# Performance work log

Measured on AMD Instinct MI355X. Metric: run time of the kernel, lower is better.

Reference implementation:

```python
import jax, jax.numpy as jnp
import numpy as np
import math

N = 50000        # nodes
DEG = 16         # regular out-degree -> E = N*DEG edges, grouped by source node
B = 64           # graphs in batch
F = 128          # num_node_features
H = 128          # nhid == enhid
RATIO = 0.5      # edge_ratio
NUM_CONVS = 3
E = N * DEG


def setup_inputs() -> dict:
    key = jax.random.key(0)
    ks = jax.random.split(key, 18)
    s = 0.05
    x = jax.random.normal(ks[0], (N, F), jnp.float32)
    edge_src = jnp.repeat(jnp.arange(N, dtype=jnp.int32), DEG)          # sorted by src
    edge_dst = jax.random.randint(ks[1], (E,), 0, N, jnp.int32)
    batch = ((jnp.arange(N) * B) // N).astype(jnp.int32)                 # sorted graph ids
    edge_attr = jnp.ones((E, 1), jnp.float32)                            # edge_attr=None branch
    inp = {"x": x, "edge_attr": edge_attr, "edge_src": edge_src,
           "edge_dst": edge_dst, "batch": batch}
    # GCNConv weights: [F->H, H->H, H->H]
    inp["W_gcn0"] = jax.random.normal(ks[2], (F, H), jnp.float32) * s
    inp["b_gcn0"] = jnp.zeros((H,), jnp.float32)
    inp["W_gcn1"] = jax.random.normal(ks[3], (H, H), jnp.float32) * s
    inp["b_gcn1"] = jnp.zeros((H,), jnp.float32)
    inp["W_gcn2"] = jax.random.normal(ks[4], (H, H), jnp.float32) * s
    inp["b_gcn2"] = jnp.zeros((H,), jnp.float32)
    # EGNN edge convs: [1->H, H->H]
    inp["W_eg0"] = jax.random.normal(ks[5], (1, H), jnp.float32) * s
    inp["b_eg0"] = jnp.zeros((H,), jnp.float32)
    inp["W_eg1"] = jax.random.normal(ks[6], (H, H), jnp.float32) * s
    inp["b_eg1"] = jnp.zeros((H,), jnp.float32)
    # score convs: [H->1, H->1]
    inp["W_sc0"] = jax.random.normal(ks[7], (H, 1), jnp.float32) * s
    inp["b_sc0"] = jnp.zeros((1,), jnp.float32)
    inp["W_sc1"] = jax.random.normal(ks[8], (H, 1), jnp.float32) * s
    inp["b_sc1"] = jnp.zeros((1,), jnp.float32)
    return inp


def _gcn(x, src, dst, ew, W, b):
    # PyG GCNConv: add self-loops (weight 1), symmetric deg normalization, aggregate at dst.
    n = x.shape[0]
    loop = jnp.arange(n, dtype=src.dtype)
    src2 = jnp.concatenate([src, loop])
    dst2 = jnp.concatenate([dst, loop])
    ew2 = jnp.concatenate([ew, jnp.ones((n,), ew.dtype)])
    deg = jax.ops.segment_sum(ew2, dst2, n)
    dinv = jnp.where(deg > 0, jax.lax.rsqrt(jnp.maximum(deg, 1e-12)), 0.0)
    norm = dinv[src2] * dinv[dst2] * ew2                                  # [E+n]
    msg = (x @ W)[src2] * norm[:, None]                                    # gather + scale
    return jax.ops.segment_sum(msg, dst2, n) + b                           # scatter-add


def _egnn(e, src, W, b):
    # Edge conv: scatter edge features to their source node, gather back, linear map.
    agg = jax.ops.segment_sum(e, src, N)
    return agg[src] @ W + b


def _pool(h, batch):
    gmax = jax.ops.segment_max(h, batch, B)
    gsum = jax.ops.segment_sum(h, batch, B)
    cnt = jax.ops.segment_sum(jnp.ones((h.shape[0],), h.dtype), batch, B)
    gmean = gsum / cnt[:, None]
    return jnp.concatenate([gmax, gmean, gsum], axis=1)                    # [B, 3H]


def reference(x, edge_attr, edge_src, edge_dst, batch,
              W_gcn0, b_gcn0, W_gcn1, b_gcn1, W_gcn2, b_gcn2,
              W_eg0, b_eg0, W_eg1, b_eg1, W_sc0, b_sc0, W_sc1, b_sc1):
    gW = [W_gcn0, W_gcn1, W_gcn2]
    gb = [b_gcn0, b_gcn1, b_gcn2]
    eW = [W_eg0, W_eg1]
    eb = [b_eg0, b_eg1]
    sW = [W_sc0, W_sc1]
    sb = [b_sc0, b_sc1]
    src, dst = edge_src, edge_dst
    deg = DEG
    ew = jnp.ones((src.shape[0],), jnp.float32)
    h = x
    ea = edge_attr
    xs = jnp.zeros((B, 3 * H), jnp.float32)
    for i in range(NUM_CONVS):
        h = jax.nn.relu(_gcn(h, src, dst, ew, gW[i], gb[i]))
        if i < NUM_CONVS - 1:
            ea = jax.nn.relu(_egnn(ea, src, eW[i], eb[i]))
            score = jnp.tanh(_egnn(ea, src, sW[i], sb[i])[:, 0])           # [E_cur]
            k = math.ceil(RATIO * deg)                                      # per-src-node top-k
            vals, idx = jax.lax.top_k(score.reshape(N, deg), k)             # [N,k]
            dst = jnp.take_along_axis(dst.reshape(N, deg), idx, axis=1).reshape(-1)
            flat = (jnp.arange(N)[:, None] * deg + idx).reshape(-1)
            ea = ea[flat]
            src = jnp.repeat(jnp.arange(N, dtype=src.dtype), k)
            ew = jnp.clip(vals.reshape(-1), 0.0, 1.0)
            deg = k
        xs = xs + _pool(h, batch)
    return xs
```

## Files before the change

### kernel.cpp

```cpp
#include <hip/hip_runtime.h>
#include <math.h>

#define NNODES 50000
#define DEGREE 16
#define NGRAPH 64
#define CAP 64
#define LDA 136
#define NXCD 8
#define XRANGE (NNODES / NXCD)
#define NTILE 782

typedef unsigned short u16;
typedef unsigned int u32;
typedef unsigned long long u64;
using short8 = __attribute__((ext_vector_type(8))) short;
using f32x4  = __attribute__((ext_vector_type(4))) float;
using fv4    = __attribute__((ext_vector_type(4))) float;
using u16x4  = __attribute__((ext_vector_type(4))) unsigned short;

__device__ __forceinline__ u16 f2bf(float f) {
  union { float f; u32 u; } v; v.f = f;
  u32 u = v.u;
  return (u16)((u + 0x7FFFu + ((u >> 16) & 1u)) >> 16);
}
__device__ __forceinline__ float2 bf2x2(u32 u) {
  union { u32 u; float f; } lo, hi;
  lo.u = (u & 0xFFFFu) << 16; hi.u = u & 0xFFFF0000u;
  return make_float2(lo.f, hi.f);
}
__device__ __forceinline__ u32 pack2(float x, float y) {
  return (u32)f2bf(x) | ((u32)f2bf(y) << 16);
}
__device__ __forceinline__ int lowerb(const int* b, int n, int v) {
  int lo = 0, hi = n;
  while (lo < hi) { int m = (lo + hi) >> 1; if (b[m] < v) lo = m + 1; else hi = m; }
  return lo;
}

__global__ __launch_bounds__(256) void k_init(
    const float* __restrict__ eattr, const float* __restrict__ x,
    const float* __restrict__ weg, const float* __restrict__ beg,
    const float* __restrict__ wsc, const float* __restrict__ bsc,
    const float* __restrict__ W0, const float* __restrict__ W1,
    const float* __restrict__ W2, const float* __restrict__ W3,
    float* __restrict__ ew1, float* __restrict__ agg0,
    u16* __restrict__ xb, u16* __restrict__ Wt,
    const int* __restrict__ edst, int* __restrict__ cnt,
    int* __restrict__ slots) {
  int b = blockIdx.x, t = threadIdx.x;
  if (b < 6250) {
    int i = b * 256 + t;
    fv4 v = __builtin_nontemporal_load(&reinterpret_cast<const fv4*>(x)[i]);
    u16x4 o = {f2bf(v.x), f2bf(v.y), f2bf(v.z), f2bf(v.w)};
    reinterpret_cast<u16x4*>(xb)[i] = o;
    if (i < NNODES) {
      const fv4* p = reinterpret_cast<const fv4*>(eattr + (size_t)i * DEGREE);
      float s = 0.f;
#pragma unroll
      for (int j = 0; j < 4; ++j) {
        fv4 w = __builtin_nontemporal_load(&p[j]);
        s += w.x + w.y + w.z + w.w;
      }
      agg0[i] = s;
      float sc = 0.f;
      for (int k = 0; k < 128; ++k) {
        float e = fmaxf(fmaf(s, weg[k], beg[k]), 0.f);
        sc = fmaf(e, wsc[k], sc);
      }
      float v1 = tanhf(fmaf(16.f, sc, bsc[0]));
      ew1[i] = fminf(fmaxf(v1, 0.f), 1.f);
    }
  } else if (b < 6506) {
    int idx = (b - 6250) * 256 + t;
    int which = idx >> 14, r = idx & 16383;
    int k = r >> 7, n = r & 127;
    const float* W = which == 0 ? W0 : which == 1 ? W1 : which == 2 ? W2 : W3;
    Wt[which * 16384 + n * 128 + k] = f2bf(W[k * 128 + n]);
  } else {
    int kk = b - 6506;
    int r = kk & (NXCD - 1);
    int bi = kk >> 3;
    int rlo = r * XRANGE, rhi = rlo + XRANGE;
    int tid = bi * 256 + t;
    for (int e = tid; e < NNODES * DEGREE; e += 128 * 256) {
      int d = __builtin_nontemporal_load(&edst[e]);
      if (d >= rlo && d < rhi) {
        int pos = atomicAdd(&cnt[d], 1);
        if (pos < CAP) slots[(size_t)d * CAP + pos] = e;
      }
    }
  }
}

__global__ __launch_bounds__(256) void k_gemmF(
    int nGemm, const u16* __restrict__ A, const u16* __restrict__ WtA,
    u16* __restrict__ outA,
    int nEg, const float* __restrict__ agg0, const float* __restrict__ weg,
    const float* __restrict__ beg, const u16* __restrict__ WtE,
    const float* __restrict__ beE, const float* __restrict__ wsc1,
    const float* __restrict__ bs1, float* __restrict__ ewOut) {
  __shared__ u16 Bs[128 * LDA];
  __shared__ u16 As[64 * LDA];
  int b = blockIdx.x, t = threadIdx.x;
  int eg = (b >= nGemm);
  const u16* Wsrc = eg ? WtE : WtA;
  for (int i = t; i < 2048; i += 256) {
    int r = i >> 4, c = (i & 15) << 3;
    *reinterpret_cast<uint4*>(&Bs[r * LDA + c]) =
        *reinterpret_cast<const uint4*>(&Wsrc[r * 128 + c]);
  }
  int m0 = (eg ? (b - nGemm) : b) * 64;
  if (eg) {
    for (int idx = t; idx < 64 * 128; idx += 256) {
      int r = idx >> 7, k = idx & 127;
      int row = m0 + r;
      float a = (row < NNODES) ? agg0[row] : 0.f;
      float v = 8.f * fmaxf(fmaf(a, weg[k], beg[k]), 0.f);
      As[r * LDA + k] = f2bf(v);
    }
  } else {
    for (int i = t; i < 1024; i += 256) {
      int r = i >> 4, c = (i & 15) << 3;
      int row = m0 + r;
      uint4 v = make_uint4(0u, 0u, 0u, 0u);
      if (row < NNODES) v = *reinterpret_cast<const uint4*>(&A[(size_t)row * 128 + c]);
      *reinterpret_cast<uint4*>(&As[r * LDA + c]) = v;
    }
  }
  __syncthreads();
  int wave = t >> 6, lane = t & 63;
  int lm = lane & 15, quad = lane >> 4;
  f32x4 z = {0.f, 0.f, 0.f, 0.f};
  f32x4 acc[8];
#pragma unroll
  for (int n = 0; n < 8; ++n) acc[n] = z;
  const u16* arow = &As[(wave * 16 + lm) * LDA + quad * 8];
#pragma unroll
  for (int kc = 0; kc < 4; ++kc) {
    short8 af = *reinterpret_cast<const short8*>(arow + kc * 32);
#pragma unroll
    for (int n = 0; n < 8; ++n) {
      short8 bf = *reinterpret_cast<const short8*>(
          &Bs[(n * 16 + lm) * LDA + kc * 32 + quad * 8]);
      acc[n] = __builtin_amdgcn_mfma_f32_16x16x32_bf16(af, bf, acc[n], 0, 0, 0);
    }
  }
  if (!eg) {
#pragma unroll
    for (int n = 0; n < 8; ++n) {
      int col = n * 16 + lm;
#pragma unroll
      for (int r = 0; r < 4; ++r) {
        int row = m0 + wave * 16 + quad * 4 + r;
        if (row < NNODES) outA[(size_t)row * 128 + col] = f2bf(acc[n][r]);
      }
    }
  } else {
    float s0 = 0.f, s1 = 0.f, s2 = 0.f, s3 = 0.f;
#pragma unroll
    for (int n = 0; n < 8; ++n) {
      int col = n * 16 + lm;
      float bb = beE[col], wv = wsc1[col];
      s0 = fmaf(fmaxf(acc[n][0] + bb, 0.f), wv, s0);
      s1 = fmaf(fmaxf(acc[n][1] + bb, 0.f), wv, s1);
      s2 = fmaf(fmaxf(acc[n][2] + bb, 0.f), wv, s2);
      s3 = fmaf(fmaxf(acc[n][3] + bb, 0.f), wv, s3);
    }
#pragma unroll
    for (int m = 8; m >= 1; m >>= 1) {
      s0 += __shfl_xor(s0, m, 64);
      s1 += __shfl_xor(s1, m, 64);
      s2 += __shfl_xor(s2, m, 64);
      s3 += __shfl_xor(s3, m, 64);
    }
    if (lm == 0) {
      float bsv = bs1[0];
      float sv[4] = {s0, s1, s2, s3};
#pragma unroll
      for (int r = 0; r < 4; ++r) {
        int row = m0 + wave * 16 + quad * 4 + r;
        if (row < NNODES) {
          float v = tanhf(fmaf(8.f, sv[r], bsv));
          ewOut[row] = fminf(fmaxf(v, 0.f), 1.f);
        }
      }
    }
  }
}

__global__ __launch_bounds__(256) void k_dinv2(
    const int* __restrict__ cnt, const int* __restrict__ slots,
    const float* __restrict__ ew1, float* __restrict__ dinv1,
    float* __restrict__ wsrc1,
    const float* __restrict__ ew2, float* __restrict__ dinv2,
    float* __restrict__ wsrc2) {
  int n = (int)((blockIdx.x * blockDim.x + threadIdx.x) >> 6);
  int lane = threadIdx.x & 63;
  if (n >= NNODES) return;
  int c = min(cnt[n], CAP);
  u32 ent = 0;
  if (lane < c) ent = (u32)slots[(size_t)n * CAP + lane];
  u32 j = ent & 15u;
  int src = (int)(ent >> 4);
  float e1 = 0.f, e2 = 0.f;
  if (lane < c && j < 8u) {
    e1 = ew1[src];
    if (j < 4u) e2 = ew2[src];
  }
#pragma unroll
  for (int m = 32; m >= 1; m >>= 1) {
    e1 += __shfl_xor(e1, m, 64);
    e2 += __shfl_xor(e2, m, 64);
  }
  float d1 = rsqrtf(1.0f + e1);
  float d2 = rsqrtf(1.0f + e2);
  if (lane == 0) {
    dinv1[n] = d1; wsrc1[n] = d1 * ew1[n];
    dinv2[n] = d2; wsrc2[n] = d2 * ew2[n];
  }
}

__global__ __launch_bounds__(256) void k_aggp(
    int nAgg, const u16* __restrict__ xwb, const int* __restrict__ cnt,
    const int* __restrict__ slots, const float* __restrict__ wsrc,
    const float* __restrict__ dinv, const float* __restrict__ bias,
    u16* __restrict__ hout, int keep, int l0mode,
    const u16* __restrict__ hpool, const int* __restrict__ batch,
    float* __restrict__ out, int poolAdd) {
  __shared__ float P[16 * 64];
  int b = blockIdx.x, t = threadIdx.x;
  int lane = t & 63;
  if (b < nAgg) {
    int n = (b * 256 + t) >> 6;
    if (n >= NNODES) return;
    int c = min(cnt[n], CAP);
    u32 e = 0;
    if (lane < c) e = (u32)slots[(size_t)n * CAP + lane];
    int kc; u32 ce;
    if (keep < 16) {
      bool valid = (lane < c) && ((e & 15u) < (u32)keep);
      u64 mask = __ballot(valid);
      kc = (int)__popcll(mask);
      u64 lt = ((u64)1 << lane) - 1;
      int pos = valid ? (int)__popcll(mask & lt) : 63 - (int)__popcll((~mask) & lt);
      ce = (u32)__builtin_amdgcn_ds_permute(pos << 2, (int)e);
    } else { kc = c; ce = e; }
    int sl = 0; float wl = 0.f;
    if (lane < kc) {
      sl = (int)(ce >> 4);
      wl = l0mode ? rsqrtf(1.0f + (float)min(cnt[sl], CAP)) : wsrc[sl];
    }
    const u32* base = reinterpret_cast<const u32*>(xwb);
    float2 acc = make_float2(0.f, 0.f);
    int i = 0;
    for (; i + 8 <= kc; i += 8) {
      u32 r[8]; float w[8];
#pragma unroll
      for (int j = 0; j < 8; ++j) {
        int s = __shfl(sl, i + j, 64);
        w[j] = __shfl(wl, i + j, 64);
        r[j] = base[(size_t)s * 64 + lane];
      }
#pragma unroll
      for (int j = 0; j < 8; ++j) {
        float2 v = bf2x2(r[j]);
        acc.x = fmaf(w[j], v.x, acc.x);
        acc.y = fmaf(w[j], v.y, acc.y);
      }
    }
    for (; i + 4 <= kc; i += 4) {
      u32 r[4]; float w[4];
#pragma unroll
      for (int j = 0; j < 4; ++j) {
        int s = __shfl(sl, i + j, 64);
        w[j] = __shfl(wl, i + j, 64);
        r[j] = base[(size_t)s * 64 + lane];
      }
#pragma unroll
      for (int j = 0; j < 4; ++j) {
        float2 v = bf2x2(r[j]);
        acc.x = fmaf(w[j], v.x, acc.x);
        acc.y = fmaf(w[j], v.y, acc.y);
      }
    }
    for (; i < kc; ++i) {
      int s = __shfl(sl, i, 64);
      float w = __shfl(wl, i, 64);
      float2 v = bf2x2(base[(size_t)s * 64 + lane]);
      acc.x = fmaf(w, v.x, acc.x);
      acc.y = fmaf(w, v.y, acc.y);
    }
    float di = l0mode ? rsqrtf(1.0f + (float)c) : dinv[n];
    float2 self = bf2x2(base[(size_t)n * 64 + lane]);
    float2 bv = reinterpret_cast<const float2*>(bias)[lane];
    float rx = fmaxf(fmaf(di, acc.x, fmaf(di * di, self.x, bv.x)), 0.f);
    float ry = fmaxf(fmaf(di, acc.y, fmaf(di * di, self.y, bv.y)), 0.f);
    reinterpret_cast<u32*>(hout + (size_t)n * 128)[lane] = pack2(rx, ry);
  } else {
    int g = b - nAgg;
    int rg = t >> 6;
    int lo = lowerb(batch, NNODES, g);
    int hi = lowerb(batch, NNODES, g + 1);
    const u32* hb = reinterpret_cast<const u32*>(hpool);
    float mxx = 0.f, mxy = 0.f, smx = 0.f, smy = 0.f;
    int n = lo + rg;
    for (; n + 28 < hi; n += 32) {
      u32 r[8];
#pragma unroll
      for (int jj = 0; jj < 8; ++jj) r[jj] = hb[(size_t)(n + 4 * jj) * 64 + lane];
#pragma unroll
      for (int jj = 0; jj < 8; ++jj) {
        float2 v = bf2x2(r[jj]);
        mxx = fmaxf(mxx, v.x); mxy = fmaxf(mxy, v.y);
        smx += v.x; smy += v.y;
      }
    }
    for (; n < hi; n += 4) {
      float2 v = bf2x2(hb[(size_t)n * 64 + lane]);
      mxx = fmaxf(mxx, v.x); mxy = fmaxf(mxy, v.y);
      smx += v.x; smy += v.y;
    }
    P[(rg * 4 + 0) * 64 + lane] = mxx;
    P[(rg * 4 + 1) * 64 + lane] = mxy;
    P[(rg * 4 + 2) * 64 + lane] = smx;
    P[(rg * 4 + 3) * 64 + lane] = smy;
    __syncthreads();
    if (t < 64) {
      float amx = 0.f, amy = 0.f, asx = 0.f, asy = 0.f;
#pragma unroll
      for (int rgi = 0; rgi < 4; ++rgi) {
        amx = fmaxf(amx, P[(rgi * 4 + 0) * 64 + t]);
        amy = fmaxf(amy, P[(rgi * 4 + 1) * 64 + t]);
        asx += P[(rgi * 4 + 2) * 64 + t];
        asy += P[(rgi * 4 + 3) * 64 + t];
      }
      float cf = (float)(hi - lo);
      int f0 = 2 * t;
      float* og = out + g * 384;
      if (poolAdd) {
        og[f0] += amx;             og[f0 + 1] += amy;
        og[128 + f0] += asx / cf;  og[128 + f0 + 1] += asy / cf;
        og[256 + f0] += asx;       og[256 + f0 + 1] += asy;
      } else {
        og[f0] = amx;              og[f0 + 1] = amy;
        og[128 + f0] = asx / cf;   og[128 + f0 + 1] = asy / cf;
        og[256 + f0] = asx;        og[256 + f0 + 1] = asy;
      }
    }
  }
}

extern "C" void kernel_launch(void* const* d_in, const int* in_sizes, int n_in,
                              void* d_out, int out_size, void* d_ws, size_t ws_size,
                              hipStream_t stream) {
  const float* x     = (const float*)d_in[0];
  const float* eattr = (const float*)d_in[1];
  const int*   edst  = (const int*)d_in[3];
  const int*   batch = (const int*)d_in[4];
  const float* Wg0 = (const float*)d_in[5];  const float* bg0 = (const float*)d_in[6];
  const float* Wg1 = (const float*)d_in[7];  const float* bg1 = (const float*)d_in[8];
  const float* Wg2 = (const float*)d_in[9];  const float* bg2 = (const float*)d_in[10];
  const float* We0 = (const float*)d_in[11]; const float* be0 = (const float*)d_in[12];
  const float* We1 = (const float*)d_in[13]; const float* be1 = (const float*)d_in[14];
  const float* Ws0 = (const float*)d_in[15]; const float* bs0 = (const float*)d_in[16];
  const float* Ws1 = (const float*)d_in[17]; const float* bs1 = (const float*)d_in[18];
  float* out = (float*)d_out;

  char* ws = (char*)d_ws;
  const size_t NBH = (size_t)NNODES * 128 * 2;
  size_t off = 0;
  auto alloc = [&](size_t bytes) { void* p = ws + off; off = (off + bytes + 255) & ~(size_t)255; return p; };
  u16*   Xb    = (u16*)alloc(NBH);
  u16*   XWb   = (u16*)alloc(NBH);
  u16*   Hb0   = (u16*)alloc(NBH);
  u16*   Hb1   = (u16*)alloc(NBH);
  u16*   Hb2   = (u16*)alloc(NBH);
  u16*   Wtb   = (u16*)alloc(4 * 128 * 128 * 2);
  int*   slots = (int*)alloc((size_t)NNODES * CAP * 4);
  int*   cnt   = (int*)alloc((size_t)NNODES * 4);
  float* agg0  = (float*)alloc((size_t)NNODES * 4);
  float* ew1   = (float*)alloc((size_t)NNODES * 4);
  float* ew2   = (float*)alloc((size_t)NNODES * 4);
  float* dinv1 = (float*)alloc((size_t)NNODES * 4);
  float* wsrc1 = (float*)alloc((size_t)NNODES * 4);
  float* dinv2 = (float*)alloc((size_t)NNODES * 4);
  float* wsrc2 = (float*)alloc((size_t)NNODES * 4);

  hipMemsetAsync(cnt, 0, (size_t)NNODES * 4, stream);
  k_init<<<7530, 256, 0, stream>>>(eattr, x, We0, be0, Ws0, bs0,
                                   Wg0, Wg1, Wg2, We1, ew1, agg0, Xb, Wtb,
                                   edst, cnt, slots);
  k_gemmF<<<2 * NTILE, 256, 0, stream>>>(
      NTILE, Xb, Wtb, XWb,
      NTILE, agg0, We0, be0, Wtb + 3 * 16384, be1, Ws1, bs1, ew2);
  k_aggp<<<12500, 256, 0, stream>>>(12500, XWb, cnt, slots, nullptr, nullptr, bg0,
                                    Hb0, 16, 1, nullptr, batch, nullptr, 0);
  k_dinv2<<<12500, 256, 0, stream>>>(cnt, slots, ew1, dinv1, wsrc1,
                                     ew2, dinv2, wsrc2);
  k_gemmF<<<NTILE, 256, 0, stream>>>(
      NTILE, Hb0, Wtb + 16384, XWb,
      0, nullptr, nullptr, nullptr, nullptr, nullptr, nullptr, nullptr, nullptr);
  k_aggp<<<12500 + NGRAPH, 256, 0, stream>>>(12500, XWb, cnt, slots, wsrc1, dinv1,
                                             bg1, Hb1, 8, 0, Hb0, batch, out, 0);
  k_gemmF<<<NTILE, 256, 0, stream>>>(
      NTILE, Hb1, Wtb + 2 * 16384, XWb,
      0, nullptr, nullptr, nullptr, nullptr, nullptr, nullptr, nullptr, nullptr);
  k_aggp<<<12500 + NGRAPH, 256, 0, stream>>>(12500, XWb, cnt, slots, wsrc2, dinv2,
                                             bg2, Hb2, 4, 0, Hb1, batch, out, 1);
  k_aggp<<<NGRAPH, 256, 0, stream>>>(0, nullptr, cnt, slots, nullptr, nullptr,
                                     nullptr, nullptr, 0, 0, Hb2, batch, out, 1);
}
```

Measured before the change: 336.0 us.

## Bucket edges by destination range in LDS before CSR slot fill

The inverse-adjacency build used to have each of 128 blocks per XCD range scan all edges and keep only those in its range, so every block read the whole edge list. Now each k_init block reads one 784-edge chunk once and sorts it in shared memory into 8 buckets by destination range. Each bucket is written to a global staging buffer, and a new k_fillB kernel does the atomic slot inserts grouped by range. This trades the redundant edge reads for an extra kernel launch and a staging write and read, and slot order still depends on atomic timing.

After: 335.6 us, median of 2. About the same (-0.1%).

```diff
diff --git a/kernel.cpp b/kernel.cpp
--- a/kernel.cpp
+++ b/kernel.cpp
@@ -9,6 +9,8 @@
 #define NXCD 8
 #define XRANGE (NNODES / NXCD)
 #define NTILE 782
+#define ACHUNK 784
+#define BCAP 192
 
 typedef unsigned short u16;
 typedef unsigned int u32;
@@ -46,7 +48,9 @@
     float* __restrict__ ew1, float* __restrict__ agg0,
     u16* __restrict__ xb, u16* __restrict__ Wt,
     const int* __restrict__ edst, int* __restrict__ cnt,
-    int* __restrict__ slots) {
+    int* __restrict__ slots, int2* __restrict__ stag, int* __restrict__ scnt) {
+  __shared__ int2 lbuf[NXCD * BCAP];
+  __shared__ int lcnt[NXCD];
   int b = blockIdx.x, t = threadIdx.x;
   if (b < 6250) {
     int i = b * 256 + t;
@@ -77,17 +81,48 @@
     const float* W = which == 0 ? W0 : which == 1 ? W1 : which == 2 ? W2 : W3;
     Wt[which * 16384 + n * 128 + k] = f2bf(W[k * 128 + n]);
   } else {
-    int kk = b - 6506;
-    int r = kk & (NXCD - 1);
-    int bi = kk >> 3;
-    int rlo = r * XRANGE, rhi = rlo + XRANGE;
-    int tid = bi * 256 + t;
-    for (int e = tid; e < NNODES * DEGREE; e += 128 * 256) {
-      int d = __builtin_nontemporal_load(&edst[e]);
-      if (d >= rlo && d < rhi) {
-        int pos = atomicAdd(&cnt[d], 1);
-        if (pos < CAP) slots[(size_t)d * CAP + pos] = e;
-      }
+    int b2 = b - 6506;
+    if (t < NXCD) lcnt[t] = 0;
+    __syncthreads();
+    int e0 = b2 * ACHUNK;
+    for (int k = 0; k < ACHUNK; k += 256) {
+      int idx = k + t;
+      int e = e0 + idx;
+      if (idx < ACHUNK && e < NNODES * DEGREE) {
+        int d = edst[e];
+        u32 r = (u32)d / (u32)XRANGE;
+        int pos = atomicAdd(&lcnt[r], 1);
+        if (pos < BCAP) {
+          lbuf[r * BCAP + pos] = make_int2(e, d);
+        } else {
+          int gp = atomicAdd(&cnt[d], 1);
+          if (gp < CAP) slots[(size_t)d * CAP + gp] = e;
+        }
+      }
+    }
+    __syncthreads();
+    for (int idx = t; idx < NXCD * BCAP; idx += 256) {
+      int r = idx / BCAP, i = idx - r * BCAP;
+      if (i < min(lcnt[r], BCAP))
+        stag[((size_t)r * 1024 + b2) * BCAP + i] = lbuf[idx];
+    }
+    if (t < NXCD) scnt[t * 1024 + b2] = min(lcnt[t], BCAP);
+  }
+}
+
+__global__ __launch_bounds__(256) void k_fillB(
+    const int2* __restrict__ stag, const int* __restrict__ scnt,
+    int* __restrict__ cnt, int* __restrict__ slots) {
+  int kk = blockIdx.x;
+  int r = kk & (NXCD - 1), sub = kk >> 3;
+  for (int q = 0; q < 8; ++q) {
+    int sb = sub * 8 + q;
+    int c = scnt[r * 1024 + sb];
+    const int2* src = &stag[((size_t)r * 1024 + sb) * BCAP];
+    for (int i = threadIdx.x; i < c; i += 256) {
+      int2 v = src[i];
+      int pos = atomicAdd(&cnt[v.y], 1);
+      if (pos < CAP) slots[(size_t)v.y * CAP + pos] = v.x;
     }
   }
 }
@@ -378,6 +413,8 @@
   u16*   Wtb   = (u16*)alloc(4 * 128 * 128 * 2);
   int*   slots = (int*)alloc((size_t)NNODES * CAP * 4);
   int*   cnt   = (int*)alloc((size_t)NNODES * 4);
+  int2*  stag  = (int2*)alloc((size_t)NXCD * 1024 * BCAP * 8);
+  int*   scnt  = (int*)alloc((size_t)NXCD * 1024 * 4);
   float* agg0  = (float*)alloc((size_t)NNODES * 4);
   float* ew1   = (float*)alloc((size_t)NNODES * 4);
   float* ew2   = (float*)alloc((size_t)NNODES * 4);
@@ -389,7 +426,8 @@
   hipMemsetAsync(cnt, 0, (size_t)NNODES * 4, stream);
   k_init<<<7530, 256, 0, stream>>>(eattr, x, We0, be0, Ws0, bs0,
                                    Wg0, Wg1, Wg2, We1, ew1, agg0, Xb, Wtb,
-                                   edst, cnt, slots);
+                                   edst, cnt, slots, stag, scnt);
+  k_fillB<<<1024, 256, 0, stream>>>(stag, scnt, cnt, slots);
   k_gemmF<<<2 * NTILE, 256, 0, stream>>>(
       NTILE, Xb, Wtb, XWb,
       NTILE, agg0, We0, be0, Wtb + 3 * 16384, be1, Ws1, bs1, ew2);
```
